# Kernel optimization log

Measured on AMD Instinct MI355X. Metric: run time of the kernel, lower is better.

The kernel has to match this reference:

```python
import jax, jax.numpy as jnp
import numpy as np

B, T, D = 2048, 200, 128


def setup_inputs() -> dict:
    key = jax.random.key(0)
    ks = jax.random.split(key, 6)
    query = jax.random.normal(ks[0], (B, D), dtype=jnp.float32)
    keys = jax.random.normal(ks[1], (B, T, D), dtype=jnp.float32)
    mask = jax.random.randint(ks[2], (B, T), 0, 2).astype(jnp.bool_)
    # nn.Linear(4D, D): weight [D, 4D], bias [D]
    lim1 = 1.0 / np.sqrt(4 * D)
    w1 = jax.random.uniform(ks[3], (D, 4 * D), minval=-lim1, maxval=lim1, dtype=jnp.float32)
    b1 = jnp.zeros((D,), dtype=jnp.float32)
    # PReLU single learnable slope (torch default init 0.25)
    prelu_a = jnp.asarray(0.25, dtype=jnp.float32)
    # nn.Linear(D, 1): weight [1, D] stored here as [D, 1], bias scalar
    lim2 = 1.0 / np.sqrt(D)
    w2 = jax.random.uniform(ks[4], (D, 1), minval=-lim2, maxval=lim2, dtype=jnp.float32)
    b2 = jnp.zeros((1,), dtype=jnp.float32)
    return {"query": query, "keys": keys, "mask": mask,
            "w1": w1, "b1": b1, "prelu_a": prelu_a, "w2": w2, "b2": b2}


def reference(query, keys, mask, w1, b1, prelu_a, w2, b2):
    # query: [B, D], keys: [B, T, D], mask: [B, T] bool
    q = jnp.broadcast_to(query[:, None, :], keys.shape)           # [B, T, D]
    x = jnp.concatenate([q, keys, q - keys, q * keys], axis=-1)   # [B, T, 4D]
    h = jnp.einsum('btf,df->btd', x, w1) + b1                     # [B, T, D]
    h = jnp.where(h >= 0, h, prelu_a * h)                         # PReLU
    scores = (h @ w2)[..., 0] + b2[0]                             # [B, T]
    scores = jnp.where(mask, scores, jnp.asarray(-1e9, scores.dtype))
    w = jax.nn.softmax(scores, axis=-1) * mask.astype(scores.dtype)
    w = w / jnp.maximum(w.sum(axis=-1, keepdims=True), 1e-6)
    return jnp.einsum('bt,btd->bd', w, keys)                      # [B, D]
```

## Files before the change

kernel.cpp:

```cpp
#include <hip/hip_runtime.h>
#include <hip/hip_bf16.h>

namespace {

constexpr int T  = 200;

typedef float f32x4 __attribute__((ext_vector_type(4)));
typedef short bf16x8 __attribute__((ext_vector_type(8)));
typedef unsigned int u32;
typedef u32 u32x4 __attribute__((ext_vector_type(4)));

__device__ __forceinline__ short f2bf(float f) {
  __hip_bfloat16 h = __float2bfloat16(f);
  return __builtin_bit_cast(short, h);
}
__device__ __forceinline__ float bflo2f(u32 u) { return __uint_as_float(u << 16); }
__device__ __forceinline__ float bfhi2f(u32 u) { return __uint_as_float(u & 0xFFFF0000u); }

template <int CTRL>
__device__ __forceinline__ float dpp_add(float x) {
  int y = __builtin_amdgcn_update_dpp(0, __float_as_int(x), CTRL, 0xF, 0xF, true);
  return x + __int_as_float(y);
}
__device__ __forceinline__ float sum16(float x) {
  x = dpp_add<0x121>(x); x = dpp_add<0x122>(x);
  x = dpp_add<0x124>(x); x = dpp_add<0x128>(x);
  return x;
}

constexpr int OFF_U2   = 8192;
constexpr int OFF_OUTL = 8448;
constexpr int OFF_RED  = 8960;
constexpr int SMEM_F   = 8968;

__global__ void pre_kernel(const float* __restrict__ w1, u32* __restrict__ MD,
                           float* __restrict__ sTf) {
  int idx = blockIdx.x * 256 + threadIdx.x;
  int d = idx >> 7, f = idx & 127;
  const float* r = w1 + (size_t)d * 512;
  u32 lo = (unsigned short)f2bf(r[128 + f] - r[256 + f]);
  u32 hi = (unsigned short)f2bf(r[384 + f]);
  MD[idx] = lo | (hi << 16);
  sTf[(size_t)f * 128 + d] = r[f] + r[256 + f];
}

__global__ void preU_kernel(const float* __restrict__ qg, const float* __restrict__ sTf,
                            const float* __restrict__ b1g, float* __restrict__ uall) {
  __shared__ float qs[128];
  int b = blockIdx.x, d = threadIdx.x;
  qs[d] = qg[(size_t)b * 128 + d];
  __syncthreads();
  float acc = b1g[d];
  #pragma unroll 16
  for (int f = 0; f < 128; ++f) acc += qs[f] * sTf[(size_t)f * 128 + d];
  uall[(size_t)b * 128 + d] = acc;
}

__device__ __forceinline__ bool mask_at(const void* m, int mcode, size_t i) {
  if (mcode == 0) return ((const int*)m)[i] != 0;
  if (mcode == 1) return ((const unsigned char*)m)[i] != 0;
  return ((const float*)m)[i] != 0.f;
}

__global__ __launch_bounds__(256, 2) void din_kernel(
    const float* __restrict__ qg, const float* __restrict__ keysg,
    const void* __restrict__ maskg, const float* __restrict__ w1g,
    const float* __restrict__ b1g, const float* __restrict__ pag,
    const float* __restrict__ w2g, const float* __restrict__ b2g,
    const u32* __restrict__ MD, const float* __restrict__ uall,
    int mode, float* __restrict__ outg) {
  __shared__ __align__(16) float smem[SMEM_F];
  float* u2   = smem + OFF_U2;
  float* outl = smem + OFF_OUTL;
  float* red  = smem + OFF_RED;

  const int tid  = threadIdx.x;
  const int b    = blockIdx.x;
  const int wid  = tid >> 6;
  const int lane = tid & 63;
  const int lrow = (lane >> 4) & 3;
  const int lcol = lane & 15;

  const float* qb    = qg + (size_t)b * 128;
  const float* keysB = keysg + (size_t)b * T * 128;

  int mcode;
  {
    unsigned v = ((const unsigned*)maskg)[lane];
    unsigned c0 = v & 255u, c1 = (v >> 8) & 255u, c2 = (v >> 16) & 255u, c3 = v >> 24;
    bool weird = (c0 == 0x80u) | (c0 == 0x3Fu) | (c1 == 0x80u) | (c1 == 0x3Fu) |
                 (c2 == 0x80u) | (c2 == 0x3Fu) | (c3 == 0x80u) | (c3 == 0x3Fu);
    bool nz = (v & 0xFFFFFF00u) != 0u;
    unsigned long long bw = __ballot(weird);
    unsigned long long bn = __ballot(nz);
    mcode = bw ? 2 : (bn ? 1 : 0);
  }

  const float pa  = pag[0];
  const float b2v = b2g[0];

  f32x4 ka0[4], ka1[4], kb0[4], kb1[4];
  #define LOADK(K0, K1, TILE)                                        \
    do {                                                             \
      int trow_ = (TILE) * 16 + lcol;                                \
      int trc_  = trow_ < T ? trow_ : T - 1;                         \
      const float* kr_ = keysB + (size_t)trc_ * 128 + lrow * 8;      \
      _Pragma("unroll")                                              \
      for (int ks = 0; ks < 4; ++ks) {                               \
        K0[ks] = *(const f32x4*)(kr_ + ks * 32);                     \
        K1[ks] = *(const f32x4*)(kr_ + ks * 32 + 4);                 \
      }                                                              \
    } while (0)

  LOADK(ka0, ka1, wid);
  LOADK(kb0, kb1, wid + 4);

  unsigned long long mw0, mw1, mw2, mw3;
  {
    size_t base = (size_t)b * T;
    bool v0 = mask_at(maskg, mcode, base + lane);
    bool v1 = mask_at(maskg, mcode, base + 64 + lane);
    bool v2 = mask_at(maskg, mcode, base + 128 + lane);
    bool v3 = (192 + lane < T) ? mask_at(maskg, mcode, base + 192 + lane) : false;
    mw0 = __ballot(v0); mw1 = __ballot(v1); mw2 = __ballot(v2); mw3 = __ballot(v3);
  }

  if (mode >= 1) {
    #pragma unroll
    for (int i = 0; i < 8; ++i) {
      int e = i * 2048 + tid * 8;
      int d = e >> 7, f = e & 127;
      u32x4 A = *(const u32x4*)(MD + e);
      u32x4 B = *(const u32x4*)(MD + e + 4);
      f32x4 q0 = *(const f32x4*)(qb + f), q1 = *(const f32x4*)(qb + f + 4);
      bf16x8 v;
      v[0] = f2bf(bflo2f(A.x) + bfhi2f(A.x) * q0.x);
      v[1] = f2bf(bflo2f(A.y) + bfhi2f(A.y) * q0.y);
      v[2] = f2bf(bflo2f(A.z) + bfhi2f(A.z) * q0.z);
      v[3] = f2bf(bflo2f(A.w) + bfhi2f(A.w) * q0.w);
      v[4] = f2bf(bflo2f(B.x) + bfhi2f(B.x) * q1.x);
      v[5] = f2bf(bflo2f(B.y) + bfhi2f(B.y) * q1.y);
      v[6] = f2bf(bflo2f(B.z) + bfhi2f(B.z) * q1.z);
      v[7] = f2bf(bflo2f(B.w) + bfhi2f(B.w) * q1.w);
      int slot = (f >> 3) ^ (d & 15);
      *(bf16x8*)((char*)smem + d * 256 + slot * 16) = v;
    }
  } else {
    #pragma unroll
    for (int i = 0; i < 8; ++i) {
      int e = i * 2048 + tid * 8;
      int d = e >> 7, f = e & 127;
      const float* r = w1g + (size_t)d * 512;
      f32x4 bB0 = *(const f32x4*)(r + 128 + f), bB1 = *(const f32x4*)(r + 128 + f + 4);
      f32x4 cC0 = *(const f32x4*)(r + 256 + f), cC1 = *(const f32x4*)(r + 256 + f + 4);
      f32x4 dd0 = *(const f32x4*)(r + 384 + f), dd1 = *(const f32x4*)(r + 384 + f + 4);
      f32x4 q0 = *(const f32x4*)(qb + f), q1 = *(const f32x4*)(qb + f + 4);
      bf16x8 v;
      v[0] = f2bf(bB0.x - cC0.x + dd0.x * q0.x);
      v[1] = f2bf(bB0.y - cC0.y + dd0.y * q0.y);
      v[2] = f2bf(bB0.z - cC0.z + dd0.z * q0.z);
      v[3] = f2bf(bB0.w - cC0.w + dd0.w * q0.w);
      v[4] = f2bf(bB1.x - cC1.x + dd1.x * q1.x);
      v[5] = f2bf(bB1.y - cC1.y + dd1.y * q1.y);
      v[6] = f2bf(bB1.z - cC1.z + dd1.z * q1.z);
      v[7] = f2bf(bB1.w - cC1.w + dd1.w * q1.w);
      int slot = (f >> 3) ^ (d & 15);
      *(bf16x8*)((char*)smem + d * 256 + slot * 16) = v;
    }
  }

  if (mode == 2) {
    if (tid < 128) u2[tid] = uall[(size_t)b * 128 + tid];
    else if (tid < 256) u2[tid] = 0.f;
  } else {
    int d = tid & 127, fh = tid >> 7;
    const float* arow = w1g + (size_t)d * 512 + fh * 64;
    const float* crow = arow + 256;
    const float* qh   = qb + fh * 64;
    float acc = 0.f;
    #pragma unroll
    for (int i = 0; i < 16; ++i) {
      f32x4 qv = *(const f32x4*)(qh + i * 4);
      f32x4 av = *(const f32x4*)(arow + i * 4);
      f32x4 cv = *(const f32x4*)(crow + i * 4);
      acc += qv.x * (av.x + cv.x) + qv.y * (av.y + cv.y) +
             qv.z * (av.z + cv.z) + qv.w * (av.w + cv.w);
    }
    if (fh == 0) acc += b1g[d];
    u2[fh * 128 + d] = acc;
  }

  __syncthreads();

  float w2w[8];
  #pragma unroll
  for (int dt = 0; dt < 8; ++dt) w2w[dt] = w2g[dt * 16 + lcol];

  float m_w = -1e9f, den_w = 0.f;
  float accpv[32];
  #pragma unroll
  for (int i = 0; i < 32; ++i) accpv[i] = 0.f;

  #define COMPUTE(TILE, K0, K1)                                              \
    do {                                                                     \
      const int tile_ = (TILE);                                              \
      bf16x8 af[4];                                                          \
      _Pragma("unroll")                                                      \
      for (int ks = 0; ks < 4; ++ks) {                                       \
        af[ks][0] = f2bf(K0[ks].x); af[ks][1] = f2bf(K0[ks].y);              \
        af[ks][2] = f2bf(K0[ks].z); af[ks][3] = f2bf(K0[ks].w);              \
        af[ks][4] = f2bf(K1[ks].x); af[ks][5] = f2bf(K1[ks].y);              \
        af[ks][6] = f2bf(K1[ks].z); af[ks][7] = f2bf(K1[ks].w);              \
      }                                                                      \
      float sj[4] = {0.f, 0.f, 0.f, 0.f};                                    \
      __builtin_amdgcn_s_setprio(1);                                         \
      _Pragma("unroll")                                                      \
      for (int dt = 0; dt < 8; ++dt) {                                       \
        int d_ = dt * 16 + lcol;                                             \
        float u_d = u2[d_] + u2[128 + d_];                                   \
        f32x4 acc = {u_d, u_d, u_d, u_d};            \
        _Pragma("unroll")                                                    \
        for (int ks = 0; ks < 4; ++ks) {                                     \
          bf16x8 bfv = *(const bf16x8*)((const char*)smem + d_ * 256 +       \
                                        (((ks * 4 + lrow) ^ (d_ & 15)) << 4)); \
          acc = __builtin_amdgcn_mfma_f32_16x16x32_bf16(af[ks], bfv, acc, 0, 0, 0); \
        }                                                                    \
        float w2d = w2w[dt];                                                 \
        _Pragma("unroll")                                                    \
        for (int j = 0; j < 4; ++j) {                                        \
          float h = acc[j];                                                  \
          h = (h >= 0.f) ? h : pa * h;                                       \
          sj[j] += h * w2d;                                                  \
        }                                                                    \
      }                                                                      \
      __builtin_amdgcn_s_setprio(0);                                         \
      _Pragma("unroll")                                                      \
      for (int j = 0; j < 4; ++j) sj[j] = sum16(sj[j]);                      \
      unsigned long long mword = tile_ < 4 ? mw0 : tile_ < 8 ? mw1           \
                                 : tile_ < 12 ? mw2 : mw3;                   \
      float mt = -1e30f;                                                     \
      _Pragma("unroll")                                                      \
      for (int j = 0; j < 4; ++j) {                                          \
        int bitp = ((tile_ & 3) << 4) + lrow * 4 + j;                        \
        bool valid = (mword >> bitp) & 1ull;                                 \
        sj[j] = valid ? (sj[j] + b2v) : -1e30f;                              \
        mt = fmaxf(mt, sj[j]);                                               \
      }                                                                      \
      mt = fmaxf(mt, __shfl_xor(mt, 16));                                    \
      mt = fmaxf(mt, __shfl_xor(mt, 32));                                    \
      if (mt > m_w + 8.f) {       \
        float sc = __expf(m_w - mt);                                         \
        den_w *= sc;                                                         \
        _Pragma("unroll")                                                    \
        for (int i = 0; i < 32; ++i) accpv[i] *= sc;                         \
        m_w = mt;                                                            \
      }                                                                      \
      float wj[4], dsum = 0.f;                                               \
      _Pragma("unroll")                                                      \
      for (int j = 0; j < 4; ++j) { wj[j] = __expf(sj[j] - m_w); dsum += wj[j]; } \
      dsum += __shfl_xor(dsum, 16);                                          \
      dsum += __shfl_xor(dsum, 32);                                          \
      den_w += dsum;                                                         \
      float tmp = (lcol & 2) ? ((lcol & 1) ? wj[3] : wj[2])                  \
                             : ((lcol & 1) ? wj[1] : wj[0]);                 \
      float wtr = __shfl(tmp, ((lcol >> 2) << 4) | (lcol & 3), 64);          \
      _Pragma("unroll")                                                      \
      for (int ks = 0; ks < 4; ++ks) {                                       \
        accpv[ks * 8 + 0] += wtr * K0[ks].x;                                 \
        accpv[ks * 8 + 1] += wtr * K0[ks].y;                                 \
        accpv[ks * 8 + 2] += wtr * K0[ks].z;                                 \
        accpv[ks * 8 + 3] += wtr * K0[ks].w;                                 \
        accpv[ks * 8 + 4] += wtr * K1[ks].x;                                 \
        accpv[ks * 8 + 5] += wtr * K1[ks].y;                                 \
        accpv[ks * 8 + 6] += wtr * K1[ks].z;                                 \
        accpv[ks * 8 + 7] += wtr * K1[ks].w;                                 \
      }                                                                      \
    } while (0)

  COMPUTE(wid, ka0, ka1);
  LOADK(ka0, ka1, wid + 8);
  COMPUTE(wid + 4, kb0, kb1);
  if (wid == 0) LOADK(kb0, kb1, 12);
  COMPUTE(wid + 8, ka0, ka1);
  if (wid == 0) COMPUTE(12, kb0, kb1);

  #pragma unroll
  for (int i = 0; i < 32; ++i) accpv[i] = sum16(accpv[i]);
  if (lcol == 0) {
    #pragma unroll
    for (int ks = 0; ks < 4; ++ks) {
      f32x4 a = {accpv[ks * 8 + 0], accpv[ks * 8 + 1], accpv[ks * 8 + 2], accpv[ks * 8 + 3]};
      f32x4 c = {accpv[ks * 8 + 4], accpv[ks * 8 + 5], accpv[ks * 8 + 6], accpv[ks * 8 + 7]};
      *(f32x4*)(outl + wid * 128 + ks * 32 + lrow * 8)     = a;
      *(f32x4*)(outl + wid * 128 + ks * 32 + lrow * 8 + 4) = c;
    }
  }
  if (lane == 0) { red[wid] = m_w; red[4 + wid] = den_w; }

  __syncthreads();

  if (tid < 128) {
    float M = fmaxf(fmaxf(red[0], red[1]), fmaxf(red[2], red[3]));
    float den = 0.f, o = 0.f;
    #pragma unroll
    for (int w = 0; w < 4; ++w) {
      float scw = __expf(red[w] - M);
      den += red[4 + w] * scw;
      o   += outl[w * 128 + tid] * scw;
    }
    float inv = (den > 0.f) ? 1.0f / den : 0.f;
    outg[(size_t)b * 128 + tid] = o * inv;
  }
  #undef COMPUTE
  #undef LOADK
}

}

extern "C" void kernel_launch(void* const* d_in, const int* in_sizes, int n_in,
                              void* d_out, int out_size, void* d_ws, size_t ws_size,
                              hipStream_t stream) {
  (void)in_sizes; (void)n_in; (void)out_size;
  const float* q    = (const float*)d_in[0];
  const float* keys = (const float*)d_in[1];
  const void*  mask = d_in[2];
  const float* w1   = (const float*)d_in[3];
  const float* b1   = (const float*)d_in[4];
  const float* pa   = (const float*)d_in[5];
  const float* w2   = (const float*)d_in[6];
  const float* b2   = (const float*)d_in[7];
  float* out = (float*)d_out;

  u32* MD     = (u32*)d_ws;
  float* sTf  = (float*)((char*)d_ws + 65536);
  float* uall = (float*)((char*)d_ws + 131072);
  int mode = 0;
  if (ws_size >= (size_t)131072 + (size_t)2048 * 128 * 4) mode = 2;
  else if (ws_size >= (size_t)131072)                     mode = 1;

  if (mode >= 1) pre_kernel<<<64, 256, 0, stream>>>(w1, MD, sTf);
  if (mode == 2) preU_kernel<<<2048, 128, 0, stream>>>(q, sTf, b1, uall);
  din_kernel<<<2048, 256, 0, stream>>>(q, keys, mask, w1, b1, pa, w2, b2,
                                       MD, uall, mode, out);
}
```

Before: 74.21 us.

## Batch preU over 8 rows, template din_kernel on mode, defer second key load

preU_kernel now handles 8 batch rows per block, so each sTf element read from global memory is reused across 8 query rows and far fewer blocks are launched. din_kernel is templated on mode, which removes runtime branches and skips the second u2 half in mode 2. The second key tile load moves after the weight-to-LDS staging, which lowers register pressure during that phase but may reduce overlap between the key load and that work.

Result: no change. 75.16 us, median of 2 (+1.3%).

```diff
diff --git a/kernel.cpp b/kernel.cpp
--- a/kernel.cpp
+++ b/kernel.cpp
@@ -46,14 +46,23 @@
 
 __global__ void preU_kernel(const float* __restrict__ qg, const float* __restrict__ sTf,
                             const float* __restrict__ b1g, float* __restrict__ uall) {
-  __shared__ float qs[128];
-  int b = blockIdx.x, d = threadIdx.x;
-  qs[d] = qg[(size_t)b * 128 + d];
+  __shared__ float qs[8][128];
+  int b0 = blockIdx.x * 8, d = threadIdx.x;
+  #pragma unroll
+  for (int r = 0; r < 8; ++r) qs[r][d] = qg[(size_t)(b0 + r) * 128 + d];
   __syncthreads();
-  float acc = b1g[d];
-  #pragma unroll 16
-  for (int f = 0; f < 128; ++f) acc += qs[f] * sTf[(size_t)f * 128 + d];
-  uall[(size_t)b * 128 + d] = acc;
+  float acc[8];
+  float bv = b1g[d];
+  #pragma unroll
+  for (int r = 0; r < 8; ++r) acc[r] = bv;
+  #pragma unroll 8
+  for (int f = 0; f < 128; ++f) {
+    float sv = sTf[(size_t)f * 128 + d];
+    #pragma unroll
+    for (int r = 0; r < 8; ++r) acc[r] += qs[r][f] * sv;
+  }
+  #pragma unroll
+  for (int r = 0; r < 8; ++r) uall[(size_t)(b0 + r) * 128 + d] = acc[r];
 }
 
 __device__ __forceinline__ bool mask_at(const void* m, int mcode, size_t i) {
@@ -62,13 +71,14 @@
   return ((const float*)m)[i] != 0.f;
 }
 
+template <int MODE>
 __global__ __launch_bounds__(256, 2) void din_kernel(
     const float* __restrict__ qg, const float* __restrict__ keysg,
     const void* __restrict__ maskg, const float* __restrict__ w1g,
     const float* __restrict__ b1g, const float* __restrict__ pag,
     const float* __restrict__ w2g, const float* __restrict__ b2g,
     const u32* __restrict__ MD, const float* __restrict__ uall,
-    int mode, float* __restrict__ outg) {
+    float* __restrict__ outg) {
   __shared__ __align__(16) float smem[SMEM_F];
   float* u2   = smem + OFF_U2;
   float* outl = smem + OFF_OUTL;
@@ -113,7 +123,6 @@
     } while (0)
 
   LOADK(ka0, ka1, wid);
-  LOADK(kb0, kb1, wid + 4);
 
   unsigned long long mw0, mw1, mw2, mw3;
   {
@@ -125,7 +134,7 @@
     mw0 = __ballot(v0); mw1 = __ballot(v1); mw2 = __ballot(v2); mw3 = __ballot(v3);
   }
 
-  if (mode >= 1) {
+  if (MODE >= 1) {
     #pragma unroll
     for (int i = 0; i < 8; ++i) {
       int e = i * 2048 + tid * 8;
@@ -169,9 +178,10 @@
     }
   }
 
-  if (mode == 2) {
+  LOADK(kb0, kb1, wid + 4);
+
+  if (MODE == 2) {
     if (tid < 128) u2[tid] = uall[(size_t)b * 128 + tid];
-    else if (tid < 256) u2[tid] = 0.f;
   } else {
     int d = tid & 127, fh = tid >> 7;
     const float* arow = w1g + (size_t)d * 512 + fh * 64;
@@ -217,7 +227,7 @@
       _Pragma("unroll")                                                      \
       for (int dt = 0; dt < 8; ++dt) {                                       \
         int d_ = dt * 16 + lcol;                                             \
-        float u_d = u2[d_] + u2[128 + d_];                                   \
+        float u_d = (MODE == 2) ? u2[d_] : (u2[d_] + u2[128 + d_]);          \
         f32x4 acc = {u_d, u_d, u_d, u_d};            \
         _Pragma("unroll")                                                    \
         for (int ks = 0; ks < 4; ++ks) {                                     \
@@ -339,7 +349,15 @@
   else if (ws_size >= (size_t)131072)                     mode = 1;
 
   if (mode >= 1) pre_kernel<<<64, 256, 0, stream>>>(w1, MD, sTf);
-  if (mode == 2) preU_kernel<<<2048, 128, 0, stream>>>(q, sTf, b1, uall);
-  din_kernel<<<2048, 256, 0, stream>>>(q, keys, mask, w1, b1, pa, w2, b2,
-                                       MD, uall, mode, out);
-}
+  if (mode == 2) preU_kernel<<<256, 128, 0, stream>>>(q, sTf, b1, uall);
+
+  if (mode == 2)
+    din_kernel<2><<<2048, 256, 0, stream>>>(q, keys, mask, w1, b1, pa, w2, b2,
+                                            MD, uall, out);
+  else if (mode == 1)
+    din_kernel<1><<<2048, 256, 0, stream>>>(q, keys, mask, w1, b1, pa, w2, b2,
+                                            MD, uall, out);
+  else
+    din_kernel<0><<<2048, 256, 0, stream>>>(q, keys, mask, w1, b1, pa, w2, b2,
+                                            MD, uall, out);
+}
```
